# Performance work log

Hardware: AMD Instinct MI355X
Metric: run time of the kernel (lower is better)

Reference implementation:

```python
import jax, jax.numpy as jnp
import numpy as np

NEG_SLOPE = 0.2  # PyG GATConv default negative_slope


def gat_conv(x, src, dst, W, a_src, a_dst, b, concat):
    # x: [N, F_in]; src/dst: [E] edge endpoints (edge j->i means src=j, dst=i)
    N = x.shape[0]
    H, C = a_src.shape
    xp = (x @ W).reshape(N, H, C)                      # per-head projection
    al_s = jnp.einsum('nhc,hc->nh', xp, a_src)          # source attention logits
    al_d = jnp.einsum('nhc,hc->nh', xp, a_dst)          # destination attention logits
    e = jax.nn.leaky_relu(al_s[src] + al_d[dst], NEG_SLOPE)   # [E, H]
    # segment softmax over incoming edges of each destination node
    m = jax.ops.segment_max(e, dst, num_segments=N)     # [N, H]
    m = jnp.where(jnp.isfinite(m), m, jnp.zeros_like(m))
    ex = jnp.exp(e - m[dst])
    den = jax.ops.segment_sum(ex, dst, num_segments=N)  # [N, H]
    alpha = ex / (den[dst] + 1e-16)                     # [E, H]
    out = jax.ops.segment_sum(xp[src] * alpha[:, :, None], dst, num_segments=N)  # [N,H,C]
    out = out.reshape(N, H * C) if concat else out.mean(axis=1)
    return out + b


def setup_inputs() -> dict:
    key = jax.random.key(0)
    ks = jax.random.split(key, 9)
    N, E, F_in, H, C = 50000, 1600000, 128, 4, 32
    x = jax.random.normal(ks[0], (N, F_in), dtype=jnp.float32)
    edge_index = jax.random.randint(ks[1], (2, E), 0, N, dtype=jnp.int64)
    s1 = 1.0 / np.sqrt(F_in)
    s2 = 1.0 / np.sqrt(H * C)
    return {
        'x': x,
        'edge_index': edge_index,
        'W1': jax.random.normal(ks[2], (F_in, H * C), dtype=jnp.float32) * s1,
        'a_src1': jax.random.normal(ks[3], (H, C), dtype=jnp.float32) * s1,
        'a_dst1': jax.random.normal(ks[4], (H, C), dtype=jnp.float32) * s1,
        'b1': jnp.zeros((H * C,), dtype=jnp.float32),
        'W2': jax.random.normal(ks[5], (H * C, C), dtype=jnp.float32) * s2,
        'a_src2': jax.random.normal(ks[6], (1, C), dtype=jnp.float32) * s2,
        'a_dst2': jax.random.normal(ks[7], (1, C), dtype=jnp.float32) * s2,
        'b2': jnp.zeros((C,), dtype=jnp.float32),
    }


def reference(x, edge_index, W1, a_src1, a_dst1, b1, W2, a_src2, a_dst2, b2):
    N = x.shape[0]
    loops = jnp.arange(N, dtype=edge_index.dtype)
    src = jnp.concatenate([edge_index[0], loops])   # PyG default add_self_loops=True
    dst = jnp.concatenate([edge_index[1], loops])
    h = gat_conv(x, src, dst, W1, a_src1, a_dst1, b1, concat=True)
    h = jax.nn.elu(h)
    out = gat_conv(h, src, dst, W2, a_src2, a_dst2, b2, concat=False)
    return out
```

## Files before the change

kernel.cpp:

```cpp
#include <hip/hip_runtime.h>
#include <hip/hip_fp16.h>

#define NEG_SLOPE 0.2f
#define CAP 128
#define NB  64
#define GAB 192
#define SUBS 32

typedef __half half_t;

__device__ __forceinline__ float lrelu(float x) { return x >= 0.f ? x : NEG_SLOPE * x; }

__device__ __forceinline__ unsigned int f2h2(float a, float b) {
    union { unsigned int u; __half2 h; } v; v.h = __floats2half2_rn(a, b);
    return v.u;
}

__device__ __forceinline__ void fma8h(const uint4& v, float w, float* a) {
    const __half* hp = (const __half*)&v;
    #pragma unroll
    for (int j = 0; j < 8; ++j) a[j] = fmaf(w, __half2float(hp[j]), a[j]);
}

__device__ __forceinline__ bool edge_is64(const int* __restrict__ ei, int E) {
    int t = threadIdx.x & 63;
    int idx = 2 * t + 1; if (idx >= 2 * E) idx = 2 * E - 1;
    unsigned long long b = __ballot(ei[idx] != 0);
    return b == 0ULL;
}

__device__ __forceinline__ void load_edge(const int* __restrict__ ei, int E, int i,
                                          bool is64, int& s, int& d) {
    if (i < E) {
        if (is64) { const long long* e = (const long long*)ei; s = (int)e[i]; d = (int)e[E + i]; }
        else      { s = ei[i]; d = ei[E + i]; }
    } else { s = d = i - E; }
}

__global__ __launch_bounds__(256) void k_count(const int* __restrict__ ei,
        int E, int N, int shift, int* __restrict__ partials, int* __restrict__ cnt) {
    __shared__ int cnts[NB];
    int t = threadIdx.x, b = blockIdx.x;
    if (t < NB) cnts[t] = 0;
    bool is64 = edge_is64(ei, E);
    for (int i = b * 256 + t; i < N; i += GAB * 256) cnt[i] = 0;
    __syncthreads();
    int tot = E + N;
    for (int i = b * 256 + t; i < tot; i += GAB * 256) {
        int s, d; load_edge(ei, E, i, is64, s, d);
        atomicAdd(&cnts[d >> shift], 1);
    }
    __syncthreads();
    if (t < NB) partials[b * NB + t] = cnts[t];
}

__global__ __launch_bounds__(256) void k_scan(int* __restrict__ partials,
                                              int* __restrict__ bin_base) {
    __shared__ int lp[GAB * NB];
    __shared__ int tot[NB], base[NB];
    int t = threadIdx.x;
    for (int i = t; i < GAB * NB; i += 256) lp[i] = partials[i];
    __syncthreads();
    if (t < NB) {
        int run = 0;
        for (int b = 0; b < GAB; ++b) { int v = lp[b * NB + t]; lp[b * NB + t] = run; run += v; }
        tot[t] = run;
    }
    __syncthreads();
    if (t == 0) {
        int run = 0;
        for (int i = 0; i < NB; ++i) { base[i] = run; run += tot[i]; }
    }
    __syncthreads();
    if (t < NB) bin_base[t] = base[t];
    if (t == 0) bin_base[NB] = base[NB - 1] + tot[NB - 1];
    for (int i = t; i < GAB * NB; i += 256) partials[i] = lp[i] + base[i & (NB - 1)];
}

__global__ __launch_bounds__(256) void k_bin(const int* __restrict__ ei,
        int E, int N, int shift, const int* __restrict__ offsets, int2* __restrict__ binned) {
    __shared__ int cur[NB];
    int t = threadIdx.x, b = blockIdx.x;
    if (t < NB) cur[t] = offsets[b * NB + t];
    bool is64 = edge_is64(ei, E);
    __syncthreads();
    int tot = E + N;
    for (int i = b * 256 + t; i < tot; i += GAB * 256) {
        int s, d; load_edge(ei, E, i, is64, s, d);
        int pos = atomicAdd(&cur[d >> shift], 1);
        binned[pos] = make_int2(s, d);
    }
}

__global__ __launch_bounds__(256) void k_fill(const int2* __restrict__ binned,
        const int* __restrict__ bin_base, int* __restrict__ cnt, int* __restrict__ adj) {
    int t = threadIdx.x;
    int bin = blockIdx.x & (NB - 1);
    int sub = blockIdx.x >> 6;
    int lo = bin_base[bin], hi = bin_base[bin + 1];
    for (int i = lo + sub * 256 + t; i < hi; i += SUBS * 256) {
        int2 e = binned[i];
        int pos = atomicAdd(&cnt[e.y], 1);
        if (pos < CAP) adj[(size_t)e.y * CAP + pos] = e.x;
    }
}

__global__ __launch_bounds__(256) void gemm1_kernel(const float* __restrict__ x,
        const float* __restrict__ W1, const float* __restrict__ a_src,
        const float* __restrict__ a_dst, half_t* __restrict__ xp1h,
        float* __restrict__ al_s, float* __restrict__ al_d, int N) {
    __shared__ __align__(16) float ws[64 * 128];
    __shared__ __align__(16) float xst[128 * 36];
    int t = threadIdx.x;
    int row0 = blockIdx.x * 32;
    if (blockIdx.x == 0 && t < 16)
        ((uint4*)(xp1h + (size_t)N * 128))[t] = make_uint4(0, 0, 0, 0);
    #pragma unroll
    for (int ii = 0; ii < 4; ++ii) {
        int idx = t + 256 * ii;
        int r = idx >> 5, kq = idx & 31;
        int n = row0 + r;
        float4 v = make_float4(0.f, 0.f, 0.f, 0.f);
        if (n < N) v = *(const float4*)&x[(size_t)n * 128 + kq * 4];
        xst[(kq * 4 + 0) * 36 + r] = v.x;
        xst[(kq * 4 + 1) * 36 + r] = v.y;
        xst[(kq * 4 + 2) * 36 + r] = v.z;
        xst[(kq * 4 + 3) * 36 + r] = v.w;
    }
    int cg = t & 31, rg = t >> 5;
    float acc[4][4] = {};
    for (int half = 0; half < 2; ++half) {
        __syncthreads();
        const float4* wsrc = (const float4*)(W1 + half * 64 * 128);
        float4* wdst = (float4*)ws;
        #pragma unroll
        for (int ii = 0; ii < 8; ++ii) wdst[t + 256 * ii] = wsrc[t + 256 * ii];
        __syncthreads();
        #pragma unroll 4
        for (int k = 0; k < 64; ++k) {
            float4 wv = *(const float4*)&ws[k * 128 + cg * 4];
            float4 xv = *(const float4*)&xst[(half * 64 + k) * 36 + rg * 4];
            float xr[4] = {xv.x, xv.y, xv.z, xv.w};
            float wr[4] = {wv.x, wv.y, wv.z, wv.w};
            #pragma unroll
            for (int r = 0; r < 4; ++r)
                #pragma unroll
                for (int c = 0; c < 4; ++c)
                    acc[r][c] = fmaf(xr[r], wr[c], acc[r][c]);
        }
    }
    #pragma unroll
    for (int r = 0; r < 4; ++r) {
        int n = row0 + rg * 4 + r;
        if (n < N) {
            uint2 u = make_uint2(f2h2(acc[r][0], acc[r][1]), f2h2(acc[r][2], acc[r][3]));
            *(uint2*)&xp1h[(size_t)n * 128 + cg * 4] = u;
        }
    }
    float ps[4], pd[4];
    #pragma unroll
    for (int r = 0; r < 4; ++r) {
        float s = 0.f, dd = 0.f;
        #pragma unroll
        for (int c = 0; c < 4; ++c) {
            s  = fmaf(acc[r][c], a_src[cg * 4 + c], s);
            dd = fmaf(acc[r][c], a_dst[cg * 4 + c], dd);
        }
        ps[r] = s; pd[r] = dd;
    }
    #pragma unroll
    for (int m = 1; m < 8; m <<= 1) {
        #pragma unroll
        for (int r = 0; r < 4; ++r) { ps[r] += __shfl_xor(ps[r], m); pd[r] += __shfl_xor(pd[r], m); }
    }
    if ((cg & 7) == 0) {
        int head = cg >> 3;
        #pragma unroll
        for (int r = 0; r < 4; ++r) {
            int n = row0 + rg * 4 + r;
            if (n < N) { al_s[n * 4 + head] = ps[r]; al_d[n * 4 + head] = pd[r]; }
        }
    }
}

__global__ __launch_bounds__(128) void edge1_kernel(const int* __restrict__ cnt,
        const int* __restrict__ adj, const float* __restrict__ al_s,
        const float* __restrict__ al_d, const half_t* __restrict__ xp1h,
        const float* __restrict__ b1, const float* __restrict__ W2,
        const float* __restrict__ a_s2, const float* __restrict__ a_d2,
        half_t* __restrict__ xp2h, float* __restrict__ al_s2, float* __restrict__ al_d2,
        int N) {
    __shared__ int srcs[CAP];
    __shared__ float ew[CAP * 4];
    __shared__ __align__(16) float red[8 * 128];
    __shared__ float h1s[128];
    __shared__ float4 wden[2];
    int d = blockIdx.x, t = threadIdx.x;
    int deg = cnt[d]; if (deg > CAP) deg = CAP;
    float4 ex = make_float4(0.f, 0.f, 0.f, 0.f);
    int s = N;
    if (t < deg) {
        s = adj[(size_t)d * CAP + t];
        float4 as = *(const float4*)&al_s[s * 4];
        float4 ad = *(const float4*)&al_d[d * 4];
        ex.x = expf(lrelu(as.x + ad.x));
        ex.y = expf(lrelu(as.y + ad.y));
        ex.z = expf(lrelu(as.z + ad.z));
        ex.w = expf(lrelu(as.w + ad.w));
    }
    srcs[t] = s;
    float4 r = ex;
    #pragma unroll
    for (int m = 1; m < 64; m <<= 1) {
        r.x += __shfl_xor(r.x, m); r.y += __shfl_xor(r.y, m);
        r.z += __shfl_xor(r.z, m); r.w += __shfl_xor(r.w, m);
    }
    if ((t & 63) == 0) wden[t >> 6] = r;
    __syncthreads();
    float4 den = wden[0], dn1 = wden[1];
    den.x += dn1.x; den.y += dn1.y; den.z += dn1.z; den.w += dn1.w;
    float4 al = make_float4(0.f, 0.f, 0.f, 0.f);
    if (t < deg) {
        al.x = ex.x / (den.x + 1e-16f); al.y = ex.y / (den.y + 1e-16f);
        al.z = ex.z / (den.z + 1e-16f); al.w = ex.w / (den.w + 1e-16f);
    }
    *(float4*)&ew[t * 4] = al;
    __syncthreads();
    int q = t & 15, p = t >> 4, h = q >> 2;
    float a[8] = {};
    const uint4* xr = (const uint4*)xp1h;
    int rr = 0;
    for (; rr + 32 <= deg; rr += 32) {
        int i0 = rr + p, i1 = i0 + 8, i2 = i0 + 16, i3 = i0 + 24;
        uint4 v0 = xr[(size_t)srcs[i0] * 16 + q];
        uint4 v1 = xr[(size_t)srcs[i1] * 16 + q];
        uint4 v2 = xr[(size_t)srcs[i2] * 16 + q];
        uint4 v3 = xr[(size_t)srcs[i3] * 16 + q];
        float w0 = ew[i0 * 4 + h], w1 = ew[i1 * 4 + h];
        float w2 = ew[i2 * 4 + h], w3 = ew[i3 * 4 + h];
        fma8h(v0, w0, a); fma8h(v1, w1, a); fma8h(v2, w2, a); fma8h(v3, w3, a);
    }
    int degp = (deg + 15) & ~15;
    for (; rr < degp; rr += 16) {
        int i0 = rr + p, i1 = i0 + 8;
        uint4 v0 = xr[(size_t)srcs[i0] * 16 + q];
        uint4 v1 = xr[(size_t)srcs[i1] * 16 + q];
        float w0 = ew[i0 * 4 + h], w1 = ew[i1 * 4 + h];
        fma8h(v0, w0, a); fma8h(v1, w1, a);
    }
    *(float4*)&red[p * 128 + q * 8 + 0] = make_float4(a[0], a[1], a[2], a[3]);
    *(float4*)&red[p * 128 + q * 8 + 4] = make_float4(a[4], a[5], a[6], a[7]);
    __syncthreads();
    float sum = 0.f;
    #pragma unroll
    for (int pp = 0; pp < 8; ++pp) sum += red[pp * 128 + t];
    float v = sum + b1[t];
    h1s[t] = v > 0.f ? v : expm1f(v);
    __syncthreads();
    int c = t & 31, g = t >> 5;
    float part = 0.f;
    #pragma unroll 8
    for (int k = 0; k < 32; ++k)
        part = fmaf(h1s[g * 32 + k], W2[(size_t)(g * 32 + k) * 32 + c], part);
    red[t] = part;
    __syncthreads();
    if (t < 32) {
        float xv = red[t] + red[t + 32] + red[t + 64] + red[t + 96];
        xp2h[(size_t)d * 32 + t] = __float2half(xv);
        float ps = xv * a_s2[t], pd = xv * a_d2[t];
        #pragma unroll
        for (int m = 1; m < 32; m <<= 1) { ps += __shfl_xor(ps, m); pd += __shfl_xor(pd, m); }
        if (t == 0) { al_s2[d] = ps; al_d2[d] = pd; }
    }
    if (d == 0 && t < 32)
        xp2h[(size_t)N * 32 + t] = __float2half(0.f);
}

__global__ __launch_bounds__(128) void edge2_kernel(const int* __restrict__ cnt,
        const int* __restrict__ adj, const float* __restrict__ al_s,
        const float* __restrict__ al_d, const half_t* __restrict__ xp2h,
        const float* __restrict__ b2v, float* __restrict__ out, int N) {
    __shared__ int srcs[CAP];
    __shared__ float ew[CAP];
    __shared__ __align__(16) float red[32 * 32];
    __shared__ float red2[128];
    __shared__ float wden[2];
    int d = blockIdx.x, t = threadIdx.x;
    int deg = cnt[d]; if (deg > CAP) deg = CAP;
    float ex = 0.f;
    int s = N;
    if (t < deg) {
        s = adj[(size_t)d * CAP + t];
        ex = expf(lrelu(al_s[s] + al_d[d]));
    }
    srcs[t] = s;
    float r = ex;
    #pragma unroll
    for (int m = 1; m < 64; m <<= 1) r += __shfl_xor(r, m);
    if ((t & 63) == 0) wden[t >> 6] = r;
    __syncthreads();
    float den = wden[0] + wden[1];
    ew[t] = (t < deg) ? ex / (den + 1e-16f) : 0.f;
    __syncthreads();
    int q = t & 3, p = t >> 2;
    float a[8] = {};
    const uint4* xr = (const uint4*)xp2h;
    if (deg <= 32) {
        uint4 v0 = xr[(size_t)srcs[p] * 4 + q];
        fma8h(v0, ew[p], a);
    } else {
        int degp = (deg + 63) & ~63;
        for (int rr = 0; rr < degp; rr += 64) {
            int i0 = rr + p, i1 = i0 + 32;
            uint4 v0 = xr[(size_t)srcs[i0] * 4 + q];
            uint4 v1 = xr[(size_t)srcs[i1] * 4 + q];
            float w0 = ew[i0], w1 = ew[i1];
            fma8h(v0, w0, a); fma8h(v1, w1, a);
        }
    }
    *(float4*)&red[p * 32 + q * 8 + 0] = make_float4(a[0], a[1], a[2], a[3]);
    *(float4*)&red[p * 32 + q * 8 + 4] = make_float4(a[4], a[5], a[6], a[7]);
    __syncthreads();
    int c = t & 31, g = t >> 5;
    float part = 0.f;
    #pragma unroll
    for (int k = 0; k < 8; ++k) part += red[(g * 8 + k) * 32 + c];
    red2[t] = part;
    __syncthreads();
    if (t < 32) {
        float s2 = red2[t] + red2[t + 32] + red2[t + 64] + red2[t + 96];
        out[(size_t)d * 32 + t] = s2 + b2v[t];
    }
}

extern "C" void kernel_launch(void* const* d_in, const int* in_sizes, int n_in,
                              void* d_out, int out_size, void* d_ws, size_t ws_size,
                              hipStream_t stream) {
    const float* x    = (const float*)d_in[0];
    const int*   ei   = (const int*)d_in[1];
    const float* W1   = (const float*)d_in[2];
    const float* a_s1 = (const float*)d_in[3];
    const float* a_d1 = (const float*)d_in[4];
    const float* b1   = (const float*)d_in[5];
    const float* W2   = (const float*)d_in[6];
    const float* a_s2 = (const float*)d_in[7];
    const float* a_d2 = (const float*)d_in[8];
    const float* b2   = (const float*)d_in[9];
    int N = in_sizes[0] / 128;
    int E = in_sizes[1] / 2;
    float* out = (float*)d_out;

    int shift = 0;
    while (((N - 1) >> shift) >= NB) shift++;

    char* wsb = (char*)d_ws;
    size_t off = 0;
    auto alloc = [&](size_t bytes) -> void* {
        void* p = wsb + off;
        off = (off + bytes + 255) & ~(size_t)255;
        return p;
    };
    int*    cnt      = (int*)   alloc((size_t)N * 4);
    int*    adj      = (int*)   alloc((size_t)N * CAP * 4);
    int*    partials = (int*)   alloc((size_t)GAB * NB * 4);
    int*    bin_base = (int*)   alloc((size_t)(NB + 1) * 4);
    int2*   binned   = (int2*)  alloc((size_t)(E + N) * 8);
    half_t* xp1h     = (half_t*)alloc((size_t)(N + 1) * 128 * 2);
    float*  al_s1    = (float*) alloc((size_t)N * 4 * 4);
    float*  al_d1    = (float*) alloc((size_t)N * 4 * 4);
    half_t* xp2h     = (half_t*)alloc((size_t)(N + 1) * 32 * 2);
    float*  al_s2    = (float*) alloc((size_t)N * 4);
    float*  al_d2    = (float*) alloc((size_t)N * 4);

    k_count<<<GAB, 256, 0, stream>>>(ei, E, N, shift, partials, cnt);
    k_scan<<<1, 256, 0, stream>>>(partials, bin_base);
    k_bin<<<GAB, 256, 0, stream>>>(ei, E, N, shift, partials, binned);
    k_fill<<<NB * SUBS, 256, 0, stream>>>(binned, bin_base, cnt, adj);
    gemm1_kernel<<<(N + 31) / 32, 256, 0, stream>>>(x, W1, a_s1, a_d1, xp1h, al_s1, al_d1, N);
    edge1_kernel<<<N, 128, 0, stream>>>(cnt, adj, al_s1, al_d1, xp1h, b1,
                                        W2, a_s2, a_d2, xp2h, al_s2, al_d2, N);
    edge2_kernel<<<N, 128, 0, stream>>>(cnt, adj, al_s2, al_d2, xp2h, b2, out, N);
}
```

Baseline: 311.1 us.

## Enlarge gemm1 register tiles and widen per-thread gathers in edge1

gemm1 now processes 128 rows per block with an 8x8 per-thread register tile and an XOR-swizzled transposed x tile in shared memory, loading x and W1 in 64-wide K chunks. The intent is more reuse per shared-memory load and fewer blocks re-reading W1. edge1 has each thread gather 16 halves (two uint4) per neighbor row, with 8 threads per row and 16 row groups, which doubles the reduction buffer and adds a barrier before h1s is written. Risks are higher register pressure and lower occupancy in gemm1, and a longer shared-memory reduction in edge1.

After: 321.4 us. 3.3% more time.

```diff
diff --git a/kernel.cpp b/kernel.cpp
--- a/kernel.cpp
+++ b/kernel.cpp
@@ -109,75 +109,86 @@
         const float* __restrict__ W1, const float* __restrict__ a_src,
         const float* __restrict__ a_dst, half_t* __restrict__ xp1h,
         float* __restrict__ al_s, float* __restrict__ al_d, int N) {
+    __shared__ __align__(16) float xst[64 * 128];
     __shared__ __align__(16) float ws[64 * 128];
-    __shared__ __align__(16) float xst[128 * 36];
     int t = threadIdx.x;
-    int row0 = blockIdx.x * 32;
+    int row0 = blockIdx.x * 128;
     if (blockIdx.x == 0 && t < 16)
         ((uint4*)(xp1h + (size_t)N * 128))[t] = make_uint4(0, 0, 0, 0);
-    #pragma unroll
-    for (int ii = 0; ii < 4; ++ii) {
-        int idx = t + 256 * ii;
-        int r = idx >> 5, kq = idx & 31;
-        int n = row0 + r;
-        float4 v = make_float4(0.f, 0.f, 0.f, 0.f);
-        if (n < N) v = *(const float4*)&x[(size_t)n * 128 + kq * 4];
-        xst[(kq * 4 + 0) * 36 + r] = v.x;
-        xst[(kq * 4 + 1) * 36 + r] = v.y;
-        xst[(kq * 4 + 2) * 36 + r] = v.z;
-        xst[(kq * 4 + 3) * 36 + r] = v.w;
-    }
-    int cg = t & 31, rg = t >> 5;
-    float acc[4][4] = {};
-    for (int half = 0; half < 2; ++half) {
+    int cg = t & 15, rg = t >> 4;
+    float acc[8][8] = {};
+    for (int chunk = 0; chunk < 2; ++chunk) {
         __syncthreads();
-        const float4* wsrc = (const float4*)(W1 + half * 64 * 128);
-        float4* wdst = (float4*)ws;
-        #pragma unroll
-        for (int ii = 0; ii < 8; ++ii) wdst[t + 256 * ii] = wsrc[t + 256 * ii];
+        int c0 = chunk * 64;
+        #pragma unroll
+        for (int ii = 0; ii < 8; ++ii) {
+            int idx = t + 256 * ii;
+            int r = idx >> 4, kq = idx & 15;
+            int n = row0 + r;
+            float4 v = make_float4(0.f, 0.f, 0.f, 0.f);
+            if (n < N) v = *(const float4*)&x[(size_t)n * 128 + c0 + kq * 4];
+            float vv[4] = {v.x, v.y, v.z, v.w};
+            #pragma unroll
+            for (int j = 0; j < 4; ++j) {
+                int k = kq * 4 + j;
+                xst[k * 128 + (((r >> 2) ^ (k & 31)) << 2) + (r & 3)] = vv[j];
+            }
+        }
+        #pragma unroll
+        for (int ii = 0; ii < 8; ++ii) {
+            int idx = t + 256 * ii;
+            int k = idx >> 5, cq = idx & 31;
+            *(float4*)&ws[k * 128 + cq * 4] =
+                *(const float4*)&W1[(size_t)(c0 + k) * 128 + cq * 4];
+        }
         __syncthreads();
+        int g0 = rg * 2, g1 = rg * 2 + 1;
         #pragma unroll 4
         for (int k = 0; k < 64; ++k) {
-            float4 wv = *(const float4*)&ws[k * 128 + cg * 4];
-            float4 xv = *(const float4*)&xst[(half * 64 + k) * 36 + rg * 4];
-            float xr[4] = {xv.x, xv.y, xv.z, xv.w};
-            float wr[4] = {wv.x, wv.y, wv.z, wv.w};
+            int kb = k & 31;
+            float4 xv0 = *(const float4*)&xst[k * 128 + ((g0 ^ kb) << 2)];
+            float4 xv1 = *(const float4*)&xst[k * 128 + ((g1 ^ kb) << 2)];
+            float4 wv0 = *(const float4*)&ws[k * 128 + cg * 8];
+            float4 wv1 = *(const float4*)&ws[k * 128 + cg * 8 + 4];
+            float xr[8] = {xv0.x, xv0.y, xv0.z, xv0.w, xv1.x, xv1.y, xv1.z, xv1.w};
+            float wr[8] = {wv0.x, wv0.y, wv0.z, wv0.w, wv1.x, wv1.y, wv1.z, wv1.w};
             #pragma unroll
-            for (int r = 0; r < 4; ++r)
+            for (int r = 0; r < 8; ++r)
                 #pragma unroll
-                for (int c = 0; c < 4; ++c)
+                for (int c = 0; c < 8; ++c)
                     acc[r][c] = fmaf(xr[r], wr[c], acc[r][c]);
         }
     }
     #pragma unroll
-    for (int r = 0; r < 4; ++r) {
-        int n = row0 + rg * 4 + r;
+    for (int r = 0; r < 8; ++r) {
+        int n = row0 + rg * 8 + r;
         if (n < N) {
-            uint2 u = make_uint2(f2h2(acc[r][0], acc[r][1]), f2h2(acc[r][2], acc[r][3]));
-            *(uint2*)&xp1h[(size_t)n * 128 + cg * 4] = u;
-        }
-    }
-    float ps[4], pd[4];
-    #pragma unroll
-    for (int r = 0; r < 4; ++r) {
+            uint4 u = make_uint4(f2h2(acc[r][0], acc[r][1]), f2h2(acc[r][2], acc[r][3]),
+                                 f2h2(acc[r][4], acc[r][5]), f2h2(acc[r][6], acc[r][7]));
+            *(uint4*)&xp1h[(size_t)n * 128 + cg * 8] = u;
+        }
+    }
+    float ps[8], pd[8];
+    #pragma unroll
+    for (int r = 0; r < 8; ++r) {
         float s = 0.f, dd = 0.f;
         #pragma unroll
-        for (int c = 0; c < 4; ++c) {
-            s  = fmaf(acc[r][c], a_src[cg * 4 + c], s);
-            dd = fmaf(acc[r][c], a_dst[cg * 4 + c], dd);
+        for (int c = 0; c < 8; ++c) {
+            s  = fmaf(acc[r][c], a_src[cg * 8 + c], s);
+            dd = fmaf(acc[r][c], a_dst[cg * 8 + c], dd);
         }
         ps[r] = s; pd[r] = dd;
     }
     #pragma unroll
-    for (int m = 1; m < 8; m <<= 1) {
-        #pragma unroll
-        for (int r = 0; r < 4; ++r) { ps[r] += __shfl_xor(ps[r], m); pd[r] += __shfl_xor(pd[r], m); }
-    }
-    if ((cg & 7) == 0) {
-        int head = cg >> 3;
-        #pragma unroll
-        for (int r = 0; r < 4; ++r) {
-            int n = row0 + rg * 4 + r;
+    for (int m = 1; m < 4; m <<= 1) {
+        #pragma unroll
+        for (int r = 0; r < 8; ++r) { ps[r] += __shfl_xor(ps[r], m); pd[r] += __shfl_xor(pd[r], m); }
+    }
+    if ((cg & 3) == 0) {
+        int head = cg >> 2;
+        #pragma unroll
+        for (int r = 0; r < 8; ++r) {
+            int n = row0 + rg * 8 + r;
             if (n < N) { al_s[n * 4 + head] = ps[r]; al_d[n * 4 + head] = pd[r]; }
         }
     }
@@ -192,7 +203,7 @@
         int N) {
     __shared__ int srcs[CAP];
     __shared__ float ew[CAP * 4];
-    __shared__ __align__(16) float red[8 * 128];
+    __shared__ __align__(16) float red[16 * 128];
     __shared__ float h1s[128];
     __shared__ float4 wden[2];
     int d = blockIdx.x, t = threadIdx.x;
@@ -226,35 +237,37 @@
     }
     *(float4*)&ew[t * 4] = al;
     __syncthreads();
-    int q = t & 15, p = t >> 4, h = q >> 2;
-    float a[8] = {};
+    int q = t & 7, p = t >> 3, h = q >> 1;
+    float a[16] = {};
     const uint4* xr = (const uint4*)xp1h;
     int rr = 0;
     for (; rr + 32 <= deg; rr += 32) {
-        int i0 = rr + p, i1 = i0 + 8, i2 = i0 + 16, i3 = i0 + 24;
-        uint4 v0 = xr[(size_t)srcs[i0] * 16 + q];
-        uint4 v1 = xr[(size_t)srcs[i1] * 16 + q];
-        uint4 v2 = xr[(size_t)srcs[i2] * 16 + q];
-        uint4 v3 = xr[(size_t)srcs[i3] * 16 + q];
+        int i0 = rr + p, i1 = i0 + 16;
+        size_t b0 = (size_t)srcs[i0] * 16 + q * 2;
+        size_t b1a = (size_t)srcs[i1] * 16 + q * 2;
+        uint4 v0 = xr[b0], v0b = xr[b0 + 1];
+        uint4 v1 = xr[b1a], v1b = xr[b1a + 1];
         float w0 = ew[i0 * 4 + h], w1 = ew[i1 * 4 + h];
-        float w2 = ew[i2 * 4 + h], w3 = ew[i3 * 4 + h];
-        fma8h(v0, w0, a); fma8h(v1, w1, a); fma8h(v2, w2, a); fma8h(v3, w3, a);
+        fma8h(v0, w0, a); fma8h(v0b, w0, a + 8);
+        fma8h(v1, w1, a); fma8h(v1b, w1, a + 8);
     }
     int degp = (deg + 15) & ~15;
     for (; rr < degp; rr += 16) {
-        int i0 = rr + p, i1 = i0 + 8;
-        uint4 v0 = xr[(size_t)srcs[i0] * 16 + q];
-        uint4 v1 = xr[(size_t)srcs[i1] * 16 + q];
-        float w0 = ew[i0 * 4 + h], w1 = ew[i1 * 4 + h];
-        fma8h(v0, w0, a); fma8h(v1, w1, a);
-    }
-    *(float4*)&red[p * 128 + q * 8 + 0] = make_float4(a[0], a[1], a[2], a[3]);
-    *(float4*)&red[p * 128 + q * 8 + 4] = make_float4(a[4], a[5], a[6], a[7]);
+        int i0 = rr + p;
+        size_t b0 = (size_t)srcs[i0] * 16 + q * 2;
+        uint4 v0 = xr[b0], v0b = xr[b0 + 1];
+        float w0 = ew[i0 * 4 + h];
+        fma8h(v0, w0, a); fma8h(v0b, w0, a + 8);
+    }
+    #pragma unroll
+    for (int j = 0; j < 4; ++j)
+        *(float4*)&red[p * 128 + q * 16 + j * 4] = make_float4(a[j*4], a[j*4+1], a[j*4+2], a[j*4+3]);
     __syncthreads();
     float sum = 0.f;
     #pragma unroll
-    for (int pp = 0; pp < 8; ++pp) sum += red[pp * 128 + t];
+    for (int pp = 0; pp < 16; ++pp) sum += red[pp * 128 + t];
     float v = sum + b1[t];
+    __syncthreads();
     h1s[t] = v > 0.f ? v : expm1f(v);
     __syncthreads();
     int c = t & 31, g = t >> 5;
@@ -376,7 +389,7 @@
     k_scan<<<1, 256, 0, stream>>>(partials, bin_base);
     k_bin<<<GAB, 256, 0, stream>>>(ei, E, N, shift, partials, binned);
     k_fill<<<NB * SUBS, 256, 0, stream>>>(binned, bin_base, cnt, adj);
-    gemm1_kernel<<<(N + 31) / 32, 256, 0, stream>>>(x, W1, a_s1, a_d1, xp1h, al_s1, al_d1, N);
+    gemm1_kernel<<<(N + 127) / 128, 256, 0, stream>>>(x, W1, a_s1, a_d1, xp1h, al_s1, al_d1, N);
     edge1_kernel<<<N, 128, 0, stream>>>(cnt, adj, al_s1, al_d1, xp1h, b1,
                                         W2, a_s2, a_d2, xp2h, al_s2, al_d2, N);
     edge2_kernel<<<N, 128, 0, stream>>>(cnt, adj, al_s2, al_d2, xp2h, b2, out, N);
```
